# Performance work log

Hardware: AMD Instinct MI355X
Metric: run time of the kernel (lower is better)

The kernel has to match this reference:

```python
import jax, jax.numpy as jnp
import numpy as np

N_NODES = 100000
N_EDGES = 1600000
IN_DIM = 64
HID_DIM = 128
OUT_DIM = 128


def setup_inputs() -> dict:
    key = jax.random.key(0)
    ks = jax.random.split(key, 12)
    s = 0.05
    return {
        "x": jax.random.normal(ks[0], (N_NODES, IN_DIM), jnp.float32),
        "edge_index": jax.random.randint(ks[1], (2, N_EDGES), 0, N_NODES, jnp.int64),
        "edge_attr": jax.random.uniform(ks[2], (N_EDGES, 2), jnp.float32),
        # conv1 MLP: Linear(IN+2, HID) -> ReLU -> Linear(HID, HID)
        "W11": jax.random.normal(ks[3], (IN_DIM + 2, HID_DIM), jnp.float32) * s,
        "b11": jax.random.normal(ks[4], (HID_DIM,), jnp.float32) * s,
        "W12": jax.random.normal(ks[5], (HID_DIM, HID_DIM), jnp.float32) * s,
        "b12": jax.random.normal(ks[6], (HID_DIM,), jnp.float32) * s,
        # conv2 MLP: Linear(HID+2, OUT) -> ReLU -> Linear(OUT, OUT)
        "W21": jax.random.normal(ks[7], (HID_DIM + 2, OUT_DIM), jnp.float32) * s,
        "b21": jax.random.normal(ks[8], (OUT_DIM,), jnp.float32) * s,
        "W22": jax.random.normal(ks[9], (OUT_DIM, OUT_DIM), jnp.float32) * s,
        "b22": jax.random.normal(ks[10], (OUT_DIM,), jnp.float32) * s,
    }


def _gin_conv(x, edge_index, edge_attr, W1, b1, W2, b2):
    N = x.shape[0]
    loop = jnp.arange(N, dtype=edge_index.dtype)
    src = jnp.concatenate([edge_index[0], loop])  # [E+N] message sources
    dst = jnp.concatenate([edge_index[1], loop])  # [E+N] aggregation targets
    # self-loop edge_attr filled with 1.0 (PyG add_self_loops default)
    ea = jnp.concatenate([edge_attr, jnp.ones((N, edge_attr.shape[1]), edge_attr.dtype)], axis=0)
    m = jnp.concatenate([x[src], ea], axis=-1)  # [E+N, F+2] gather + concat
    h = jnp.dot(jax.nn.relu(jnp.dot(m, W1) + b1), W2) + b2  # edge MLP
    return jax.ops.segment_sum(h, dst, num_segments=N)  # scatter-add aggregate


def reference(x, edge_index, edge_attr, W11, b11, W12, b12, W21, b21, W22, b22):
    h = _gin_conv(x, edge_index, edge_attr, W11, b11, W12, b12)
    h = jax.nn.relu(h)
    return _gin_conv(h, edge_index, edge_attr, W21, b21, W22, b22)
```

## Files before the change

kernel.cpp:

```cpp
#include <hip/hip_runtime.h>


typedef unsigned int uint;
typedef __attribute__((ext_vector_type(8))) short bf16x8;
typedef __attribute__((ext_vector_type(4))) float f32x4;

#define BSHIFT 11
#define BNODES (1 << BSHIFT)

static __device__ __forceinline__ unsigned short f2bf(float f) {
    uint u = __float_as_uint(f);
    uint r = (u + 0x7fffu + ((u >> 16) & 1u)) >> 16;
    return (unsigned short)r;
}


__global__ void init_kernel(int* bcnt, int* ptr, int N, int E) {
    int i = threadIdx.x;
    if (i < 64) bcnt[i] = 0;
    if (i == 0) ptr[N] = E;
}


__global__ void wprep_all(const float* __restrict__ W11, const float* __restrict__ W12,
                          const float* __restrict__ W21, const float* __restrict__ W22,
                          unsigned short* Wt11, unsigned short* Wt12,
                          unsigned short* Wt21, unsigned short* Wt22) {
    int idx = blockIdx.x * 256 + threadIdx.x;
    const float* W; unsigned short* Wt; int K; int off;
    if (idx < 64 * 128)        { W = W11; Wt = Wt11; K = 64;  off = idx; }
    else if (idx < 192 * 128)  { W = W12; Wt = Wt12; K = 128; off = idx - 64 * 128; }
    else if (idx < 320 * 128)  { W = W21; Wt = Wt21; K = 128; off = idx - 192 * 128; }
    else if (idx < 448 * 128)  { W = W22; Wt = Wt22; K = 128; off = idx - 320 * 128; }
    else return;
    int k = off >> 7, n = off & 127;
    Wt[n * K + k] = f2bf(W[k * 128 + n]);
}


__global__ __launch_bounds__(256) void bin_kernel(
    const int* __restrict__ src, const int* __restrict__ dst,
    const float* __restrict__ ea, int* __restrict__ bcnt,
    int2* __restrict__ barr, int CAP, int E, int B) {
    __shared__ int hist[64];
    __shared__ int bbase[64];
    __shared__ int gbase[64];
    __shared__ int2 sorted[2048];
    __shared__ unsigned char bof[2048];
    const int tileBase = blockIdx.x * 2048;
    int n = E - tileBase; if (n > 2048) n = 2048; if (n <= 0) return;
    const int tid = threadIdx.x;
    if (tid < 64) hist[tid] = 0;
    __syncthreads();

    int2 ent[8]; int bk[8]; int rk[8];
#pragma unroll
    for (int k = 0; k < 8; k++) {
        int i = k * 256 + tid;
        bk[k] = -1;
        if (i < n) {
            int e = tileBase + i;
            int s = src[e], d = dst[e];
            float2 a = reinterpret_cast<const float2*>(ea)[e];
            int b = d >> BSHIFT;
            int dloc = d & (BNODES - 1);
            ent[k].x = s | (dloc << 17);
            ent[k].y = (int)((uint)f2bf(a.x) | ((uint)f2bf(a.y) << 16));
            bk[k] = b;
            rk[k] = atomicAdd(&hist[b], 1);
        }
    }
    __syncthreads();
    if (tid == 0) {
        int run = 0;
        for (int b = 0; b < B; b++) { bbase[b] = run; run += hist[b]; }
    }
    __syncthreads();
    if (tid < B && hist[tid] > 0) gbase[tid] = atomicAdd(&bcnt[tid], hist[tid]);
    __syncthreads();
#pragma unroll
    for (int k = 0; k < 8; k++) {
        if (bk[k] >= 0) {
            int p = bbase[bk[k]] + rk[k];
            sorted[p] = ent[k];
            bof[p] = (unsigned char)bk[k];
        }
    }
    __syncthreads();
    for (int i = tid; i < n; i += 256) {
        int b = bof[i];
        barr[(long)b * CAP + gbase[b] + (i - bbase[b])] = sorted[i];
    }
}


__global__ __launch_bounds__(1024) void bucket_csr(
    const int2* __restrict__ barr, const int* __restrict__ bcnt,
    int CAP, int N, int B,
    int2* __restrict__ csr, int* __restrict__ ptr) {
    __shared__ int hist[BNODES];
    __shared__ int pairs[1024];
    __shared__ int lptr[BNODES];
    const int g = blockIdx.x;
    const int tid = threadIdx.x;
    const int cnt = bcnt[g];
    int base = 0;
    for (int b = 0; b < g; b++) base += bcnt[b];

    hist[tid] = 0; hist[tid + 1024] = 0;
    __syncthreads();
    const int2* my = barr + (long)g * CAP;
    for (int i = tid; i < cnt; i += 1024) {
        int dloc = ((uint)my[i].x) >> 17;
        atomicAdd(&hist[dloc], 1);
    }
    __syncthreads();
    int ps = hist[2 * tid] + hist[2 * tid + 1];
    pairs[tid] = ps;
    __syncthreads();
    for (int off = 1; off < 1024; off <<= 1) {
        int t = (tid >= off) ? pairs[tid - off] : 0;
        __syncthreads();
        pairs[tid] += t;
        __syncthreads();
    }
    int excl = pairs[tid] - ps;
    lptr[2 * tid] = excl;
    lptr[2 * tid + 1] = excl + hist[2 * tid];
    __syncthreads();
    for (int i = tid; i < BNODES; i += 1024) {
        long gnode = (long)g * BNODES + i;
        if (gnode <= (long)N) ptr[gnode] = base + lptr[i];
    }
    __syncthreads();
    for (int i = tid; i < cnt; i += 1024) {
        int2 v = my[i];
        int dloc = ((uint)v.x) >> 17;
        int pos = base + atomicAdd(&lptr[dloc], 1);
        int2 o; o.x = v.x & 0x1FFFF; o.y = v.y;
        csr[pos] = o;
    }
}


__global__ __launch_bounds__(256) void gather_kernel(
    const uint* __restrict__ Au, const int* __restrict__ ptr,
    const int2* __restrict__ csr, const float* __restrict__ we,
    uint* __restrict__ B, int N) {
    int node = blockIdx.x * 4 + (threadIdx.x >> 6);
    if (node >= N) return;
    int t = threadIdx.x & 63;
    int c = 2 * t;
    float w0x = we[c], w0y = we[c + 1];
    float w1x = we[128 + c], w1y = we[128 + c + 1];

    const char* Ab = (const char*)Au;
    const uint t4 = (uint)t * 4u;
#define LD(sidx) (*(const uint*)(Ab + ((((uint)(sidx)) << 8) + t4)))
#define ACC(rv, ev)                                                      \
    {                                                                    \
        float a0 = __uint_as_float(((uint)(ev)) << 16);                  \
        float a1 = __uint_as_float(((uint)(ev)) & 0xffff0000u);          \
        float vx = __uint_as_float((rv) << 16);                          \
        float vy = __uint_as_float((rv) & 0xffff0000u);                  \
        vx = fmaf(a0, w0x, fmaf(a1, w1x, vx));                           \
        vy = fmaf(a0, w0y, fmaf(a1, w1y, vy));                           \
        ax += fmaxf(vx, 0.f);                                            \
        ay += fmaxf(vy, 0.f);                                            \
    }
    uint selfv = LD(node);
    float ax = fmaxf(__uint_as_float(selfv << 16) + w0x + w1x, 0.f);
    float ay = fmaxf(__uint_as_float(selfv & 0xffff0000u) + w0y + w1y, 0.f);

    int k = ptr[node], end = ptr[node + 1];
    for (; k + 8 <= end; k += 8) {
        int2 c0 = csr[k], c1 = csr[k + 1], c2 = csr[k + 2], c3 = csr[k + 3];
        int2 c4 = csr[k + 4], c5 = csr[k + 5], c6 = csr[k + 6], c7 = csr[k + 7];
        uint r0 = LD(c0.x); uint r1 = LD(c1.x); uint r2 = LD(c2.x); uint r3 = LD(c3.x);
        uint r4 = LD(c4.x); uint r5 = LD(c5.x); uint r6 = LD(c6.x); uint r7 = LD(c7.x);
        ACC(r0, c0.y) ACC(r1, c1.y) ACC(r2, c2.y) ACC(r3, c3.y)
        ACC(r4, c4.y) ACC(r5, c5.y) ACC(r6, c6.y) ACC(r7, c7.y)
    }
    for (; k + 4 <= end; k += 4) {
        int2 c0 = csr[k], c1 = csr[k + 1], c2 = csr[k + 2], c3 = csr[k + 3];
        uint r0 = LD(c0.x); uint r1 = LD(c1.x); uint r2 = LD(c2.x); uint r3 = LD(c3.x);
        ACC(r0, c0.y) ACC(r1, c1.y) ACC(r2, c2.y) ACC(r3, c3.y)
    }
    for (; k < end; k++) {
        int2 c0 = csr[k];
        uint r0 = LD(c0.x);
        ACC(r0, c0.y)
    }
#undef ACC
#undef LD
    B[(long)node * 64 + t] = (uint)f2bf(ax) | ((uint)f2bf(ay) << 16);
}


template <int K, bool IN_F32, bool OUT_BF16, bool USE_CNT, bool RELU>
__global__ __launch_bounds__(256) void gemm_mfma(
    const void* __restrict__ Ain, const unsigned short* __restrict__ Wt,
    const float* __restrict__ bias, const int* __restrict__ ptr,
    void* __restrict__ Cout, int N) {
    constexpr int KS = K / 32;
    const int wave = threadIdx.x >> 6;
    const int lane = threadIdx.x & 63;
    const int m = lane & 15, quad = lane >> 4;
    const long rowBase = (long)blockIdx.x * 64;

    bf16x8 bfrag[2][KS];
#pragma unroll
    for (int ct = 0; ct < 2; ct++) {
        int col = (wave * 2 + ct) * 16 + m;
#pragma unroll
        for (int ks = 0; ks < KS; ks++)
            bfrag[ct][ks] = *(const bf16x8*)(Wt + (long)col * K + ks * 32 + quad * 8);
    }

#pragma unroll
    for (int rt = 0; rt < 4; rt++) {
        long row = rowBase + rt * 16 + m;
        long rc = row < N ? row : (long)N - 1;
        bf16x8 afrag[KS];
        if (IN_F32) {
            const float* arow = (const float*)Ain + rc * K;
#pragma unroll
            for (int ks = 0; ks < KS; ks++) {
                float4 lo = *(const float4*)(arow + ks * 32 + quad * 8);
                float4 hi = *(const float4*)(arow + ks * 32 + quad * 8 + 4);
                bf16x8 f;
                f[0] = (short)f2bf(lo.x); f[1] = (short)f2bf(lo.y);
                f[2] = (short)f2bf(lo.z); f[3] = (short)f2bf(lo.w);
                f[4] = (short)f2bf(hi.x); f[5] = (short)f2bf(hi.y);
                f[6] = (short)f2bf(hi.z); f[7] = (short)f2bf(hi.w);
                afrag[ks] = f;
            }
        } else {
            const unsigned short* arow = (const unsigned short*)Ain + rc * K;
#pragma unroll
            for (int ks = 0; ks < KS; ks++)
                afrag[ks] = *(const bf16x8*)(arow + ks * 32 + quad * 8);
        }

#pragma unroll
        for (int ct = 0; ct < 2; ct++) {
            f32x4 acc = {0.f, 0.f, 0.f, 0.f};
#pragma unroll
            for (int ks = 0; ks < KS; ks++)
                acc = __builtin_amdgcn_mfma_f32_16x16x32_bf16(afrag[ks], bfrag[ct][ks], acc, 0, 0, 0);

            int col = (wave * 2 + ct) * 16 + m;
            float b = bias[col];
#pragma unroll
            for (int r = 0; r < 4; r++) {
                long orow = rowBase + rt * 16 + quad * 4 + r;
                if (orow < N) {
                    float v = acc[r];
                    if (USE_CNT) v += b * (float)(ptr[orow + 1] - ptr[orow] + 1);
                    else v += b;
                    if (RELU) v = fmaxf(v, 0.f);
                    if (OUT_BF16) ((unsigned short*)Cout)[orow * 128 + col] = f2bf(v);
                    else ((float*)Cout)[orow * 128 + col] = v;
                }
            }
        }
    }
}


__global__ __launch_bounds__(256) void fused_mid_gemm(
    const unsigned short* __restrict__ Bin, const int* __restrict__ ptr,
    const unsigned short* __restrict__ WtA, const float* __restrict__ biasA,
    const unsigned short* __restrict__ WtB, const float* __restrict__ biasB,
    unsigned short* __restrict__ Cout, int N) {
    __shared__ unsigned short ts[64 * 136];
    const int wave = threadIdx.x >> 6;
    const int lane = threadIdx.x & 63;
    const int m = lane & 15, quad = lane >> 4;
    const long rowBase = (long)blockIdx.x * 64;

    bf16x8 bfrag[2][4];
#pragma unroll
    for (int ct = 0; ct < 2; ct++) {
        int col = (wave * 2 + ct) * 16 + m;
#pragma unroll
        for (int ks = 0; ks < 4; ks++)
            bfrag[ct][ks] = *(const bf16x8*)(WtA + (long)col * 128 + ks * 32 + quad * 8);
    }

    f32x4 acc[4][2];
#pragma unroll
    for (int rt = 0; rt < 4; rt++) {
        long row = rowBase + rt * 16 + m;
        long rc = row < N ? row : (long)N - 1;
        const unsigned short* arow = Bin + rc * 128;
        bf16x8 af[4];
#pragma unroll
        for (int ks = 0; ks < 4; ks++)
            af[ks] = *(const bf16x8*)(arow + ks * 32 + quad * 8);
#pragma unroll
        for (int ct = 0; ct < 2; ct++) {
            f32x4 a = {0.f, 0.f, 0.f, 0.f};
#pragma unroll
            for (int ks = 0; ks < 4; ks++)
                a = __builtin_amdgcn_mfma_f32_16x16x32_bf16(af[ks], bfrag[ct][ks], a, 0, 0, 0);
            acc[rt][ct] = a;
        }
    }

#pragma unroll
    for (int rt = 0; rt < 4; rt++) {
        float cntf[4];
#pragma unroll
        for (int r = 0; r < 4; r++) {
            long grow = rowBase + rt * 16 + quad * 4 + r;
            cntf[r] = (grow < N) ? (float)(ptr[grow + 1] - ptr[grow] + 1) : 1.f;
        }
#pragma unroll
        for (int ct = 0; ct < 2; ct++) {
            int col = (wave * 2 + ct) * 16 + m;
            float b = biasA[col];
#pragma unroll
            for (int r = 0; r < 4; r++) {
                int row = rt * 16 + quad * 4 + r;
                ts[row * 136 + col] = f2bf(fmaxf(acc[rt][ct][r] + b * cntf[r], 0.f));
            }
        }
    }
    __syncthreads();

#pragma unroll
    for (int ct = 0; ct < 2; ct++) {
        int col = (wave * 2 + ct) * 16 + m;
#pragma unroll
        for (int ks = 0; ks < 4; ks++)
            bfrag[ct][ks] = *(const bf16x8*)(WtB + (long)col * 128 + ks * 32 + quad * 8);
    }
#pragma unroll
    for (int rt = 0; rt < 4; rt++) {
        const unsigned short* lr = ts + (rt * 16 + m) * 136;
        bf16x8 af[4];
#pragma unroll
        for (int ks = 0; ks < 4; ks++)
            af[ks] = *(const bf16x8*)(lr + ks * 32 + quad * 8);
#pragma unroll
        for (int ct = 0; ct < 2; ct++) {
            f32x4 a = {0.f, 0.f, 0.f, 0.f};
#pragma unroll
            for (int ks = 0; ks < 4; ks++)
                a = __builtin_amdgcn_mfma_f32_16x16x32_bf16(af[ks], bfrag[ct][ks], a, 0, 0, 0);
            int col = (wave * 2 + ct) * 16 + m;
            float b = biasB[col];
#pragma unroll
            for (int r = 0; r < 4; r++) {
                long grow = rowBase + rt * 16 + quad * 4 + r;
                if (grow < N) Cout[grow * 128 + col] = f2bf(a[r] + b);
            }
        }
    }
}


extern "C" void kernel_launch(void* const* d_in, const int* in_sizes, int n_in,
                              void* d_out, int out_size, void* d_ws, size_t ws_size,
                              hipStream_t stream) {
    const float* x   = (const float*)d_in[0];
    const int*   ei  = (const int*)d_in[1];
    const float* ea  = (const float*)d_in[2];
    const float* W11 = (const float*)d_in[3];
    const float* b11 = (const float*)d_in[4];
    const float* W12 = (const float*)d_in[5];
    const float* b12 = (const float*)d_in[6];
    const float* W21 = (const float*)d_in[7];
    const float* b21 = (const float*)d_in[8];
    const float* W22 = (const float*)d_in[9];
    const float* b22 = (const float*)d_in[10];
    float* out = (float*)d_out;

    const int N = in_sizes[0] / 64;
    const int E = in_sizes[1] / 2;
    const int* src = ei;
    const int* dst = ei + E;

    const int B = (N + BNODES - 1) >> BSHIFT;
    const int CAP = E / B + 4096;

    char* p = (char*)d_ws;
    unsigned short* A_bf = (unsigned short*)p;  p += (size_t)N * 128 * 2;
    unsigned short* B_bf = (unsigned short*)p;
    int2* barr = (int2*)B_bf;                   p += (size_t)N * 128 * 2;
    int2* csr  = (int2*)p;                      p += (size_t)E * 8;
    int* ptr   = (int*)p;                       p += (size_t)(N + 1) * 4;
    int* bcnt  = (int*)p;                       p += 64 * 4;
    unsigned short* Wt11 = (unsigned short*)p;  p += (size_t)64 * 128 * 2;
    unsigned short* Wt12 = (unsigned short*)p;  p += (size_t)128 * 128 * 2;
    unsigned short* Wt21 = (unsigned short*)p;  p += (size_t)128 * 128 * 2;
    unsigned short* Wt22 = (unsigned short*)p;

    const int binBlocks = (E + 2047) / 2048;
    const int gatherBlocks = (N + 3) / 4;
    const int tileBlocks = (N + 63) / 64;

    init_kernel<<<1, 64, 0, stream>>>(bcnt, ptr, N, E);
    wprep_all<<<(448 * 128 + 255) / 256, 256, 0, stream>>>(W11, W12, W21, W22,
                                                           Wt11, Wt12, Wt21, Wt22);

    bin_kernel<<<binBlocks, 256, 0, stream>>>(src, dst, ea, bcnt, barr, CAP, E, B);
    bucket_csr<<<B, 1024, 0, stream>>>(barr, bcnt, CAP, N, B, csr, ptr);

    gemm_mfma<64, true, true, false, false><<<tileBlocks, 256, 0, stream>>>(
        x, Wt11, b11, nullptr, A_bf, N);
    gather_kernel<<<gatherBlocks, 256, 0, stream>>>((const uint*)A_bf, ptr, csr,
                                                    W11 + 64 * 128, (uint*)B_bf, N);
    fused_mid_gemm<<<tileBlocks, 256, 0, stream>>>(B_bf, ptr, Wt12, b12, Wt21, b21, A_bf, N);
    gather_kernel<<<gatherBlocks, 256, 0, stream>>>((const uint*)A_bf, ptr, csr,
                                                    W21 + 128 * 128, (uint*)B_bf, N);
    gemm_mfma<128, false, false, true, false><<<tileBlocks, 256, 0, stream>>>(
        B_bf, Wt22, b22, ptr, out, N);
}
```

Baseline: 401.3 us.

## Halve CSR bucket width, widen bin tiles, fold init into weight prep

Shrinks destination buckets from 2048 to 1024 nodes, so the bucket CSR kernel launches about twice as many blocks, each with one node per thread and a simpler scan. The binning kernel now uses 512-thread blocks over 4096-edge tiles with up to 128 buckets. The separate init kernel is merged into the weight-prep kernel to save a launch. The gather loop reads its row bounds through readfirstlane and trades the 4-wide tail loop for a 2-wide one plus a single leftover edge.

```diff
diff --git a/kernel.cpp b/kernel.cpp
--- a/kernel.cpp
+++ b/kernel.cpp
@@ -5,7 +5,7 @@
 typedef __attribute__((ext_vector_type(8))) short bf16x8;
 typedef __attribute__((ext_vector_type(4))) float f32x4;
 
-#define BSHIFT 11
+#define BSHIFT 10
 #define BNODES (1 << BSHIFT)
 
 static __device__ __forceinline__ unsigned short f2bf(float f) {
@@ -15,18 +15,14 @@
 }
 
 
-__global__ void init_kernel(int* bcnt, int* ptr, int N, int E) {
-    int i = threadIdx.x;
-    if (i < 64) bcnt[i] = 0;
-    if (i == 0) ptr[N] = E;
-}
-
-
 __global__ void wprep_all(const float* __restrict__ W11, const float* __restrict__ W12,
                           const float* __restrict__ W21, const float* __restrict__ W22,
                           unsigned short* Wt11, unsigned short* Wt12,
-                          unsigned short* Wt21, unsigned short* Wt22) {
+                          unsigned short* Wt21, unsigned short* Wt22,
+                          int* bcnt, int* ptr, int N, int E) {
     int idx = blockIdx.x * 256 + threadIdx.x;
+    if (idx < 128) bcnt[idx] = 0;
+    if (idx == 128) ptr[N] = E;
     const float* W; unsigned short* Wt; int K; int off;
     if (idx < 64 * 128)        { W = W11; Wt = Wt11; K = 64;  off = idx; }
     else if (idx < 192 * 128)  { W = W12; Wt = Wt12; K = 128; off = idx - 64 * 128; }
@@ -38,25 +34,25 @@
 }
 
 
-__global__ __launch_bounds__(256) void bin_kernel(
+__global__ __launch_bounds__(512) void bin_kernel(
     const int* __restrict__ src, const int* __restrict__ dst,
     const float* __restrict__ ea, int* __restrict__ bcnt,
     int2* __restrict__ barr, int CAP, int E, int B) {
-    __shared__ int hist[64];
-    __shared__ int bbase[64];
-    __shared__ int gbase[64];
-    __shared__ int2 sorted[2048];
-    __shared__ unsigned char bof[2048];
-    const int tileBase = blockIdx.x * 2048;
-    int n = E - tileBase; if (n > 2048) n = 2048; if (n <= 0) return;
+    __shared__ int hist[128];
+    __shared__ int bbase[128];
+    __shared__ int gbase[128];
+    __shared__ int2 sorted[4096];
+    __shared__ unsigned char bof[4096];
+    const int tileBase = blockIdx.x * 4096;
+    int n = E - tileBase; if (n > 4096) n = 4096; if (n <= 0) return;
     const int tid = threadIdx.x;
-    if (tid < 64) hist[tid] = 0;
+    if (tid < 128) hist[tid] = 0;
     __syncthreads();
 
     int2 ent[8]; int bk[8]; int rk[8];
 #pragma unroll
     for (int k = 0; k < 8; k++) {
-        int i = k * 256 + tid;
+        int i = k * 512 + tid;
         bk[k] = -1;
         if (i < n) {
             int e = tileBase + i;
@@ -87,7 +83,7 @@
         }
     }
     __syncthreads();
-    for (int i = tid; i < n; i += 256) {
+    for (int i = tid; i < n; i += 512) {
         int b = bof[i];
         barr[(long)b * CAP + gbase[b] + (i - bbase[b])] = sorted[i];
     }
@@ -99,7 +95,7 @@
     int CAP, int N, int B,
     int2* __restrict__ csr, int* __restrict__ ptr) {
     __shared__ int hist[BNODES];
-    __shared__ int pairs[1024];
+    __shared__ int scn[BNODES];
     __shared__ int lptr[BNODES];
     const int g = blockIdx.x;
     const int tid = threadIdx.x;
@@ -107,7 +103,7 @@
     int base = 0;
     for (int b = 0; b < g; b++) base += bcnt[b];
 
-    hist[tid] = 0; hist[tid + 1024] = 0;
+    hist[tid] = 0;
     __syncthreads();
     const int2* my = barr + (long)g * CAP;
     for (int i = tid; i < cnt; i += 1024) {
@@ -115,29 +111,25 @@
         atomicAdd(&hist[dloc], 1);
     }
     __syncthreads();
-    int ps = hist[2 * tid] + hist[2 * tid + 1];
-    pairs[tid] = ps;
+    int v = hist[tid];
+    scn[tid] = v;
     __syncthreads();
     for (int off = 1; off < 1024; off <<= 1) {
-        int t = (tid >= off) ? pairs[tid - off] : 0;
+        int t = (tid >= off) ? scn[tid - off] : 0;
         __syncthreads();
-        pairs[tid] += t;
+        scn[tid] += t;
         __syncthreads();
     }
-    int excl = pairs[tid] - ps;
-    lptr[2 * tid] = excl;
-    lptr[2 * tid + 1] = excl + hist[2 * tid];
-    __syncthreads();
-    for (int i = tid; i < BNODES; i += 1024) {
-        long gnode = (long)g * BNODES + i;
-        if (gnode <= (long)N) ptr[gnode] = base + lptr[i];
-    }
+    int excl = scn[tid] - v;
+    lptr[tid] = excl;
+    long gnode = (long)g * BNODES + tid;
+    if (gnode < (long)N) ptr[gnode] = base + excl;
     __syncthreads();
     for (int i = tid; i < cnt; i += 1024) {
-        int2 v = my[i];
-        int dloc = ((uint)v.x) >> 17;
+        int2 e = my[i];
+        int dloc = ((uint)e.x) >> 17;
         int pos = base + atomicAdd(&lptr[dloc], 1);
-        int2 o; o.x = v.x & 0x1FFFF; o.y = v.y;
+        int2 o; o.x = e.x & 0x1FFFF; o.y = e.y;
         csr[pos] = o;
     }
 }
@@ -172,21 +164,23 @@
     float ax = fmaxf(__uint_as_float(selfv << 16) + w0x + w1x, 0.f);
     float ay = fmaxf(__uint_as_float(selfv & 0xffff0000u) + w0y + w1y, 0.f);
 
-    int k = ptr[node], end = ptr[node + 1];
+    int k   = __builtin_amdgcn_readfirstlane(ptr[node]);
+    int end = __builtin_amdgcn_readfirstlane(ptr[node + 1]);
+
     for (; k + 8 <= end; k += 8) {
-        int2 c0 = csr[k], c1 = csr[k + 1], c2 = csr[k + 2], c3 = csr[k + 3];
+        int2 c0 = csr[k],     c1 = csr[k + 1], c2 = csr[k + 2], c3 = csr[k + 3];
         int2 c4 = csr[k + 4], c5 = csr[k + 5], c6 = csr[k + 6], c7 = csr[k + 7];
         uint r0 = LD(c0.x); uint r1 = LD(c1.x); uint r2 = LD(c2.x); uint r3 = LD(c3.x);
         uint r4 = LD(c4.x); uint r5 = LD(c5.x); uint r6 = LD(c6.x); uint r7 = LD(c7.x);
         ACC(r0, c0.y) ACC(r1, c1.y) ACC(r2, c2.y) ACC(r3, c3.y)
         ACC(r4, c4.y) ACC(r5, c5.y) ACC(r6, c6.y) ACC(r7, c7.y)
     }
-    for (; k + 4 <= end; k += 4) {
-        int2 c0 = csr[k], c1 = csr[k + 1], c2 = csr[k + 2], c3 = csr[k + 3];
-        uint r0 = LD(c0.x); uint r1 = LD(c1.x); uint r2 = LD(c2.x); uint r3 = LD(c3.x);
-        ACC(r0, c0.y) ACC(r1, c1.y) ACC(r2, c2.y) ACC(r3, c3.y)
-    }
-    for (; k < end; k++) {
+    for (; k + 2 <= end; k += 2) {
+        int2 c0 = csr[k], c1 = csr[k + 1];
+        uint r0 = LD(c0.x); uint r1 = LD(c1.x);
+        ACC(r0, c0.y) ACC(r1, c1.y)
+    }
+    if (k < end) {
         int2 c0 = csr[k];
         uint r0 = LD(c0.x);
         ACC(r0, c0.y)
@@ -391,21 +385,20 @@
     int2* barr = (int2*)B_bf;                   p += (size_t)N * 128 * 2;
     int2* csr  = (int2*)p;                      p += (size_t)E * 8;
     int* ptr   = (int*)p;                       p += (size_t)(N + 1) * 4;
-    int* bcnt  = (int*)p;                       p += 64 * 4;
+    int* bcnt  = (int*)p;                       p += 128 * 4;
     unsigned short* Wt11 = (unsigned short*)p;  p += (size_t)64 * 128 * 2;
     unsigned short* Wt12 = (unsigned short*)p;  p += (size_t)128 * 128 * 2;
     unsigned short* Wt21 = (unsigned short*)p;  p += (size_t)128 * 128 * 2;
     unsigned short* Wt22 = (unsigned short*)p;
 
-    const int binBlocks = (E + 2047) / 2048;
+    const int binBlocks = (E + 4095) / 4096;
     const int gatherBlocks = (N + 3) / 4;
     const int tileBlocks = (N + 63) / 64;
 
-    init_kernel<<<1, 64, 0, stream>>>(bcnt, ptr, N, E);
     wprep_all<<<(448 * 128 + 255) / 256, 256, 0, stream>>>(W11, W12, W21, W22,
-                                                           Wt11, Wt12, Wt21, Wt22);
-
-    bin_kernel<<<binBlocks, 256, 0, stream>>>(src, dst, ea, bcnt, barr, CAP, E, B);
+                                                           Wt11, Wt12, Wt21, Wt22,
+                                                           bcnt, ptr, N, E);
+    bin_kernel<<<binBlocks, 512, 0, stream>>>(src, dst, ea, bcnt, barr, CAP, E, B);
     bucket_csr<<<B, 1024, 0, stream>>>(barr, bcnt, CAP, N, B, csr, ptr);
 
     gemm_mfma<64, true, true, false, false><<<tileBlocks, 256, 0, stream>>>(
```

Result: faster. 370.0 us (-7.8%).
